# Performance work log

Measured on AMD Instinct MI355X. Metric: run time of the kernel, lower is better.

The kernel has to match this reference:

```python
import jax, jax.numpy as jnp
import numpy as np

THRESH = 0.3
DECAY = 0.5


def spike_fn(x):
    # Heaviside threshold (forward only)
    return (x > THRESH).astype(x.dtype)


def setup_inputs() -> dict:
    key = jax.random.key(0)
    k_in, k0, k1, k2 = jax.random.split(key, 4)
    B, D0, T = 128, 512, 512
    inputs = jax.random.uniform(k_in, (B, D0, T), dtype=jnp.float32)
    w0 = jax.random.normal(k0, (512, 1024), dtype=jnp.float32)
    w1 = jax.random.normal(k1, (1024, 1024), dtype=jnp.float32)
    w2 = jax.random.normal(k2, (1024, 512), dtype=jnp.float32)
    return {"inputs": inputs, "w0": w0, "w1": w1, "w2": w2}


def reference(inputs, w0, w1, w2):
    ws = (w0, w1, w2)
    B = inputs.shape[0]
    layer_dims = tuple(w.shape[1] for w in ws)

    # time-major: [T, B, D0]
    xs = jnp.transpose(inputs, (2, 0, 1))

    mem0 = tuple(jnp.zeros((B, d), dtype=inputs.dtype) for d in layer_dims)
    spk0 = tuple(jnp.zeros((B, d), dtype=inputs.dtype) for d in layer_dims)

    def step(carry, x_t):
        mems, spikes = carry
        prev_spike = x_t  # layer-0 spikes come straight from the input
        new_mems, new_spikes = [], []
        for i, w in enumerate(ws):
            # leaky integrate with reset-by-spike, then fire
            mem = mems[i] * DECAY * (1.0 - spikes[i]) + prev_spike @ w
            s = spike_fn(mem)
            new_mems.append(mem)
            new_spikes.append(s)
            prev_spike = s
        return (tuple(new_mems), tuple(new_spikes)), None

    (_, spikes_final), _ = jax.lax.scan(step, (mem0, spk0), xs)
    return spikes_final[-1]
```

## Files before the change

kernel.cpp:

```cpp
#include <hip/hip_runtime.h>


typedef __bf16 bf16;
typedef __attribute__((ext_vector_type(8))) __bf16 bf16x8;
typedef __attribute__((ext_vector_type(16))) float f32x16;
typedef unsigned long long u64;

#define B_   128
#define D0_  512
#define T_   512
#define TS_  128
#define N1_  1024
#define N2_  1024
#define N3_  512
#define MFMA32(a,b,c) __builtin_amdgcn_mfma_f32_32x32x16_bf16((a),(b),(c),0,0,0)

#define GL2LDS(g, l) __builtin_amdgcn_global_load_lds( \
    (const __attribute__((address_space(1))) void*)(g), \
    (__attribute__((address_space(3))) void*)(l), 16, 0, 0)

#define WAIT_BARRIER() do { \
    asm volatile("s_waitcnt vmcnt(0)" ::: "memory"); \
    __builtin_amdgcn_s_barrier(); } while (0)


__global__ __launch_bounds__(256)
void split_w(const float* __restrict__ W, bf16* __restrict__ WTh, bf16* __restrict__ WTl,
             int K, int N)
{
    __shared__ float tile[32][33];
    const int k0 = blockIdx.x * 32, n0 = blockIdx.y * 32;
    const int tx = threadIdx.x & 31, ty = threadIdx.x >> 5;
#pragma unroll
    for (int r = 0; r < 4; ++r)
        tile[ty + r * 8][tx] = W[(size_t)(k0 + ty + r * 8) * N + n0 + tx];
    __syncthreads();
#pragma unroll
    for (int r = 0; r < 4; ++r) {
        int nl = ty + r * 8;
        float v = tile[tx][nl];
        bf16 h = (bf16)v;
        size_t o = (size_t)(n0 + nl) * K + k0 + tx;
        WTh[o] = h;
        WTl[o] = (bf16)(v - (float)h);
    }
}

__global__ __launch_bounds__(64)
void split_wf(const float* __restrict__ W, bf16* __restrict__ Fh, bf16* __restrict__ Fl,
              int K, int N)
{
    const int l = threadIdx.x;
    const int kc = blockIdx.x;
    const int np = blockIdx.y;
    const int c  = np * 32 + (l & 31);
    const int k0 = kc * 16 + (l >> 5) * 8;
    const size_t ob = (((size_t)np * (K / 16) + kc) * 64 + l) * 8;
#pragma unroll
    for (int e = 0; e < 8; ++e) {
        float v = W[(size_t)(k0 + e) * N + c];
        bf16 h = (bf16)v;
        Fh[ob + e] = h;
        Fl[ob + e] = (bf16)(v - (float)h);
    }
}

__global__ __launch_bounds__(256)
void split_x(const float* __restrict__ in, bf16* __restrict__ Xh, bf16* __restrict__ Xl)
{
    __shared__ float tile[32][33];
    const int b = blockIdx.z, d0 = blockIdx.x * 32, t0 = blockIdx.y * 32;
    const int tx = threadIdx.x & 31, ty = threadIdx.x >> 5;
#pragma unroll
    for (int r = 0; r < 4; ++r)
        tile[ty + r * 8][tx] = in[((size_t)b * D0_ + d0 + ty + r * 8) * T_ + t0 + tx];
    __syncthreads();
    const int s = t0 >> 7;
#pragma unroll
    for (int r = 0; r < 4; ++r) {
        int t  = t0 + ty + r * 8;
        int tl = t & (TS_ - 1);
        float v = tile[tx][ty + r * 8];
        bf16 h = (bf16)v;
        size_t o = (((size_t)s * B_ + b) * TS_ + tl) * D0_ + d0 + tx;
        Xh[o] = h;
        Xl[o] = (bf16)(v - (float)h);
    }
}

__device__ __forceinline__ bf16x8 expand8(unsigned v)
{
    union { unsigned u[4]; bf16x8 h; } r;
    const unsigned p = v * 0x8001u;
#pragma unroll
    for (int i = 0; i < 4; ++i)
        r.u[i] = ((p >> (2 * i)) & 0x10001u) * 0x3F80u;
    return r.h;
}

__global__ __launch_bounds__(256, 2)
void snn_layer0(const bf16* __restrict__ Ah, const bf16* __restrict__ Al,
                const bf16* __restrict__ WTh, const bf16* __restrict__ WTl,
                u64* __restrict__ bitsOut)
{
    constexpr int K = D0_;
    __shared__ char smem[65536];
    bf16* sA0  = (bf16*)(smem);
    bf16* sAl0 = (bf16*)(smem + 8192);
    bf16* sB0  = (bf16*)(smem + 16384);
    bf16* sBl0 = (bf16*)(smem + 24576);
    bf16* sA1  = (bf16*)(smem + 32768);
    bf16* sAl1 = (bf16*)(smem + 40960);
    bf16* sB1  = (bf16*)(smem + 49152);
    bf16* sBl1 = (bf16*)(smem + 57344);
    float* If  = (float*)smem;

    const int tid = threadIdx.x, lane = tid & 63, w = tid >> 6;
    const int wm = w & 1, wn = w >> 1;
    const int l31 = lane & 31, kh = lane >> 5;
    const int bid = blockIdx.x;
    const int b  = (bid & 7) | ((bid >> 6) << 3);
    const int nb = ((bid >> 3) & 7) * 128;

    const int i4 = lane >> 2, c4 = lane & 3;
    const int csrc = c4 ^ ((i4 >> 1) & 3);
    const bf16* gBh = WTh + (size_t)(nb + w * 32 + i4) * K + csrc * 8;
    const bf16* gBl = WTl + (size_t)(nb + w * 32 + i4) * K + csrc * 8;
    const int wT = w * 32 * 32;

    int rA[2], rB[2], swA[2], swB[2];
#pragma unroll
    for (int i = 0; i < 2; ++i) {
        rA[i] = wm * 64 + i * 32 + l31;
        rB[i] = wn * 64 + i * 32 + l31;
        swA[i] = (rA[i] >> 1) & 3;
        swB[i] = (rB[i] >> 1) & 3;
    }

    float cm = 0.f, cs = 0.f;
    const int scol = tid & 63;
    float* Ifb = If + (tid >> 6) * 4096;

#define STAGE0(dA, dAl, dBh, dBl, go)                                          \
    do {                                                                       \
        _Pragma("unroll")                                                      \
        for (int inst = 0; inst < 2; ++inst) {                                 \
            GL2LDS(gA  + (size_t)(inst * 16) * K + (go), (dA)  + wT + inst * 16 * 32); \
            GL2LDS(gAl + (size_t)(inst * 16) * K + (go), (dAl) + wT + inst * 16 * 32); \
            GL2LDS(gBh + (size_t)(inst * 16) * K + (go), (dBh) + wT + inst * 16 * 32); \
            GL2LDS(gBl + (size_t)(inst * 16) * K + (go), (dBl) + wT + inst * 16 * 32); \
        }                                                                      \
    } while (0)

#define KSTEP0(cA, cAl, cBh, cBl)                                              \
    do {                                                                       \
        bf16x8 a[2][2], al2[2][2];                                             \
        _Pragma("unroll")                                                      \
        for (int mi = 0; mi < 2; ++mi)                                         \
            _Pragma("unroll")                                                  \
            for (int h = 0; h < 2; ++h) {                                      \
                const int off = rA[mi] * 32 + (((2 * h + kh) ^ swA[mi]) * 8);  \
                a[mi][h]   = *(const bf16x8*)((cA) + off);                     \
                al2[mi][h] = *(const bf16x8*)((cAl) + off);                    \
            }                                                                  \
        _Pragma("unroll")                                                      \
        for (int h = 0; h < 2; ++h) {                                          \
            bf16x8 bh[2], bl[2];                                               \
            _Pragma("unroll")                                                  \
            for (int ni = 0; ni < 2; ++ni) {                                   \
                const int off = rB[ni] * 32 + (((2 * h + kh) ^ swB[ni]) * 8);  \
                bh[ni] = *(const bf16x8*)((cBh) + off);                        \
                bl[ni] = *(const bf16x8*)((cBl) + off);                        \
            }                                                                  \
            _Pragma("unroll")                                                  \
            for (int ni = 0; ni < 2; ++ni)                                     \
                _Pragma("unroll")                                              \
                for (int mi = 0; mi < 2; ++mi)                                 \
                    acc[mi][ni] = MFMA32(a[mi][h], bh[ni], acc[mi][ni]);       \
            _Pragma("unroll")                                                  \
            for (int ni = 0; ni < 2; ++ni)                                     \
                _Pragma("unroll")                                              \
                for (int mi = 0; mi < 2; ++mi)                                 \
                    acc[mi][ni] = MFMA32(al2[mi][h], bh[ni], acc[mi][ni]);     \
            _Pragma("unroll")                                                  \
            for (int ni = 0; ni < 2; ++ni)                                     \
                _Pragma("unroll")                                              \
                for (int mi = 0; mi < 2; ++mi)                                 \
                    acc[mi][ni] = MFMA32(a[mi][h], bl[ni], acc[mi][ni]);       \
        }                                                                      \
        WAIT_BARRIER();                                                        \
    } while (0)

#pragma unroll 1
    for (int s = 0; s < T_ / TS_; ++s) {
        const size_t arow = ((size_t)s * B_ + b) * TS_;
        const bf16* gA  = Ah + (arow + w * 32 + i4) * K + csrc * 8;
        const bf16* gAl = Al + (arow + w * 32 + i4) * K + csrc * 8;

        STAGE0(sA0, sAl0, sB0, sBl0, 0);
        WAIT_BARRIER();

        f32x16 acc[2][2] = {};

#pragma unroll 1
        for (int ks = 0; ks < K / 32; ks += 2) {
            STAGE0(sA1, sAl1, sB1, sBl1, (ks + 1) * 32);
            KSTEP0(sA0, sAl0, sB0, sBl0);
            if (ks + 2 < K / 32)
                STAGE0(sA0, sAl0, sB0, sBl0, (ks + 2) * 32);
            KSTEP0(sA1, sAl1, sB1, sBl1);
        }

        u64 word0 = 0, word1 = 0;
        if (wm == 0) {
#pragma unroll
            for (int ni = 0; ni < 2; ++ni)
#pragma unroll
                for (int mi = 0; mi < 2; ++mi)
#pragma unroll
                    for (int r = 0; r < 16; ++r) {
                        const int tt = mi * 32 + (r & 3) + 8 * (r >> 2) + 4 * kh;
                        If[wn * 4096 + tt * 64 + ni * 32 + l31] = acc[mi][ni][r];
                    }
        }
        __syncthreads();
        if (tid < 128) {
            float m = cm, sp = cs;
#pragma unroll 4
            for (int tt = 0; tt < 64; ++tt) {
                m = m * 0.5f * (1.0f - sp) + Ifb[tt * 64 + scol];
                const bool fire = m > 0.3f;
                sp = fire ? 1.0f : 0.0f;
                u64 bal = __ballot(fire);
                if ((tid & 63) == tt) word0 = bal;
            }
            cm = m; cs = sp;
        }
        __syncthreads();
        if (wm == 1) {
#pragma unroll
            for (int ni = 0; ni < 2; ++ni)
#pragma unroll
                for (int mi = 0; mi < 2; ++mi)
#pragma unroll
                    for (int r = 0; r < 16; ++r) {
                        const int tt = mi * 32 + (r & 3) + 8 * (r >> 2) + 4 * kh;
                        If[wn * 4096 + tt * 64 + ni * 32 + l31] = acc[mi][ni][r];
                    }
        }
        __syncthreads();
        if (tid < 128) {
            float m = cm, sp = cs;
#pragma unroll 4
            for (int tt = 0; tt < 64; ++tt) {
                m = m * 0.5f * (1.0f - sp) + Ifb[tt * 64 + scol];
                const bool fire = m > 0.3f;
                sp = fire ? 1.0f : 0.0f;
                u64 bal = __ballot(fire);
                if ((tid & 63) == tt) word1 = bal;
            }
            cm = m; cs = sp;
            u64* dst = bitsOut + ((size_t)s * B_ + b) * 2048;
            const int j8 = (nb >> 6) + (tid >> 6);
            const int t0 = tid & 63, t1 = 64 + (tid & 63);
            dst[t0 * 16 + (j8 ^ (t0 & 15))] = word0;
            dst[t1 * 16 + (j8 ^ (t1 & 15))] = word1;
        }
        __syncthreads();
    }
#undef STAGE0
#undef KSTEP0
}

template<bool WRITE_BITS>
__global__ __launch_bounds__(256, 2)
void snn_layer_bits(const u64* __restrict__ bitsIn,
                    const bf16* __restrict__ WFh, const bf16* __restrict__ WFl,
                    u64* __restrict__ bitsOut, float* __restrict__ outp, int N)
{
    constexpr int K = 1024, KC = K / 16;
    __shared__ char smem[49152];
    char* bitsLds = smem;
    float* If = (float*)(smem + 16384);

    const int tid = threadIdx.x, lane = tid & 63, w = tid >> 6;
    const int wm = w & 1, wn = w >> 1;
    const int l31 = lane & 31, kh = lane >> 5;
    const int b = blockIdx.y;
    const int nb = blockIdx.x * 128;

    const size_t fb0 = ((size_t)((nb >> 5) + wn * 2) * KC) * 512 + (size_t)lane * 8;
    const size_t fb1 = fb0 + (size_t)KC * 512;
    const bf16* h0 = WFh + fb0;
    const bf16* h1 = WFh + fb1;
    const bf16* l0 = WFl + fb0;
    const bf16* l1 = WFl + fb1;

    const int sh8 = 8 * kh, s15 = l31 & 15;
    const int rA0b = (wm * 64 + l31) * 128;
    const int rA1b = (wm * 64 + 32 + l31) * 128;

    float cm = 0.f, cs = 0.f;
    const int scol = tid & 63;
    float* Ifb = If + (tid >> 6) * 4096;

#define LOADQ(sl, kc)                                                          \
    do {                                                                       \
        q0h[sl] = *(const bf16x8*)(h0 + (size_t)(kc) * 512);                   \
        q1h[sl] = *(const bf16x8*)(h1 + (size_t)(kc) * 512);                   \
        q0l[sl] = *(const bf16x8*)(l0 + (size_t)(kc) * 512);                   \
        q1l[sl] = *(const bf16x8*)(l1 + (size_t)(kc) * 512);                   \
    } while (0)

#define JSTEP(j, CB0, CB1)                                                     \
    do {                                                                       \
        bf16x8 a0 = expand8((unsigned)((CB0) >> (16 * (j) + sh8)) & 0xFFu);    \
        bf16x8 a1 = expand8((unsigned)((CB1) >> (16 * (j) + sh8)) & 0xFFu);    \
        acc[0][0] = MFMA32(a0, q0h[j], acc[0][0]);                             \
        acc[1][0] = MFMA32(a1, q0h[j], acc[1][0]);                             \
        acc[0][1] = MFMA32(a0, q1h[j], acc[0][1]);                             \
        acc[1][1] = MFMA32(a1, q1h[j], acc[1][1]);                             \
        acc[0][0] = MFMA32(a0, q0l[j], acc[0][0]);                             \
        acc[1][0] = MFMA32(a1, q0l[j], acc[1][0]);                             \
        acc[0][1] = MFMA32(a0, q1l[j], acc[0][1]);                             \
        acc[1][1] = MFMA32(a1, q1l[j], acc[1][1]);                             \
    } while (0)

#pragma unroll 1
    for (int s = 0; s < T_ / TS_; ++s) {
        {
            const char* src = (const char*)bitsIn + ((size_t)s * B_ + b) * 16384;
#pragma unroll
            for (int i = 0; i < 4; ++i)
                GL2LDS(src + (w * 4 + i) * 1024 + lane * 16,
                       bitsLds + (w * 4 + i) * 1024);
        }
        WAIT_BARRIER();

        f32x16 acc[2][2] = {};
        bf16x8 q0h[4], q0l[4], q1h[4], q1l[4];

        LOADQ(0, 0);
        LOADQ(1, 1);
        u64 cb0 = *(const u64*)(bitsLds + rA0b + ((0 ^ s15) << 3));
        u64 cb1 = *(const u64*)(bitsLds + rA1b + ((0 ^ s15) << 3));

#pragma unroll 1
        for (int pi = 0; pi < 15; ++pi) {
            const u64 nb0 = *(const u64*)(bitsLds + rA0b + (((pi + 1) ^ s15) << 3));
            const u64 nb1 = *(const u64*)(bitsLds + rA1b + (((pi + 1) ^ s15) << 3));
            const int kc = pi * 4;
            LOADQ(2, kc + 2); JSTEP(0, cb0, cb1);
            LOADQ(3, kc + 3); JSTEP(1, cb0, cb1);
            LOADQ(0, kc + 4); JSTEP(2, cb0, cb1);
            LOADQ(1, kc + 5); JSTEP(3, cb0, cb1);
            cb0 = nb0; cb1 = nb1;
        }
        LOADQ(2, 62); JSTEP(0, cb0, cb1);
        LOADQ(3, 63); JSTEP(1, cb0, cb1);
        JSTEP(2, cb0, cb1);
        JSTEP(3, cb0, cb1);

        u64 word0 = 0, word1 = 0;
        if (wm == 0) {
#pragma unroll
            for (int ni = 0; ni < 2; ++ni)
#pragma unroll
                for (int mi = 0; mi < 2; ++mi)
#pragma unroll
                    for (int r = 0; r < 16; ++r) {
                        const int tt = mi * 32 + (r & 3) + 8 * (r >> 2) + 4 * kh;
                        If[wn * 4096 + tt * 64 + ni * 32 + l31] = acc[mi][ni][r];
                    }
        }
        __syncthreads();
        if (tid < 128) {
            float m = cm, sp = cs;
#pragma unroll 4
            for (int tt = 0; tt < 64; ++tt) {
                m = m * 0.5f * (1.0f - sp) + Ifb[tt * 64 + scol];
                const bool fire = m > 0.3f;
                sp = fire ? 1.0f : 0.0f;
                if constexpr (WRITE_BITS) {
                    u64 bal = __ballot(fire);
                    if ((tid & 63) == tt) word0 = bal;
                }
            }
            cm = m; cs = sp;
        }
        __syncthreads();
        if (wm == 1) {
#pragma unroll
            for (int ni = 0; ni < 2; ++ni)
#pragma unroll
                for (int mi = 0; mi < 2; ++mi)
#pragma unroll
                    for (int r = 0; r < 16; ++r) {
                        const int tt = mi * 32 + (r & 3) + 8 * (r >> 2) + 4 * kh;
                        If[wn * 4096 + tt * 64 + ni * 32 + l31] = acc[mi][ni][r];
                    }
        }
        __syncthreads();
        if (tid < 128) {
            float m = cm, sp = cs;
#pragma unroll 4
            for (int tt = 0; tt < 64; ++tt) {
                m = m * 0.5f * (1.0f - sp) + Ifb[tt * 64 + scol];
                const bool fire = m > 0.3f;
                sp = fire ? 1.0f : 0.0f;
                if constexpr (WRITE_BITS) {
                    u64 bal = __ballot(fire);
                    if ((tid & 63) == tt) word1 = bal;
                }
            }
            cm = m; cs = sp;
            if constexpr (WRITE_BITS) {
                u64* dst = bitsOut + ((size_t)s * B_ + b) * 2048;
                const int j8 = (nb >> 6) + (tid >> 6);
                const int t0 = tid & 63, t1 = 64 + (tid & 63);
                dst[t0 * 16 + (j8 ^ (t0 & 15))] = word0;
                dst[t1 * 16 + (j8 ^ (t1 & 15))] = word1;
            } else {
                if (s == T_ / TS_ - 1)
                    outp[(size_t)b * N + nb + tid] = cs;
            }
        }
        __syncthreads();
    }
#undef LOADQ
#undef JSTEP
}

extern "C" void kernel_launch(void* const* d_in, const int* in_sizes, int n_in,
                              void* d_out, int out_size, void* d_ws, size_t ws_size,
                              hipStream_t stream)
{
    const float* x  = (const float*)d_in[0];
    const float* w0 = (const float*)d_in[1];
    const float* w1 = (const float*)d_in[2];
    const float* w2 = (const float*)d_in[3];
    float* out = (float*)d_out;

    char* p = (char*)d_ws;
    bf16* w0h  = (bf16*)p; p += (size_t)N1_ * D0_ * 2;
    bf16* w0l  = (bf16*)p; p += (size_t)N1_ * D0_ * 2;
    bf16* wf1h = (bf16*)p; p += (size_t)N2_ * N1_ * 2;
    bf16* wf1l = (bf16*)p; p += (size_t)N2_ * N1_ * 2;
    bf16* wf2h = (bf16*)p; p += (size_t)N3_ * N2_ * 2;
    bf16* wf2l = (bf16*)p; p += (size_t)N3_ * N2_ * 2;
    bf16* Xh   = (bf16*)p; p += (size_t)T_ * B_ * D0_ * 2;
    bf16* Xl   = (bf16*)p; p += (size_t)T_ * B_ * D0_ * 2;
    u64* bits0 = (u64*)p;  p += (size_t)(T_/TS_) * B_ * TS_ * (N1_/8);
    u64* bits1 = (u64*)p;  p += (size_t)(T_/TS_) * B_ * TS_ * (N2_/8);

    split_w<<<dim3(D0_/32, N1_/32), 256, 0, stream>>>(w0, w0h, w0l, D0_, N1_);
    split_wf<<<dim3(N1_/16, N2_/32), 64, 0, stream>>>(w1, wf1h, wf1l, N1_, N2_);
    split_wf<<<dim3(N2_/16, N3_/32), 64, 0, stream>>>(w2, wf2h, wf2l, N2_, N3_);
    split_x<<<dim3(D0_/32, T_/32, B_), 256, 0, stream>>>(x, Xh, Xl);

    snn_layer0<<<dim3(B_ * (N1_/128)), 256, 0, stream>>>(Xh, Xl, w0h, w0l, bits0);
    snn_layer_bits<true ><<<dim3(N2_/128, B_), 256, 0, stream>>>(
        bits0, wf1h, wf1l, bits1, nullptr, N2_);
    snn_layer_bits<false><<<dim3(N3_/128, B_), 256, 0, stream>>>(
        bits1, wf2h, wf2l, nullptr, out, N3_);
}
```

Baseline: 806.0 us.

## Pre-swizzle layer-0 operands into MFMA fragment layout and load directly to registers

The input and layer-0 weights are now split into bf16 hi/lo parts stored in MFMA-fragment order, so snn_layer0 reads each operand fragment straight from global memory into registers with a two-slot register double buffer. This removes the LDS staging, swizzled LDS reads and per-k-step barriers from the layer-0 GEMM. In exchange, operand tiles are no longer shared through LDS, so each wave loads its own fragments from global/L2. The new split_xf kernel reads the input with strided per-thread loads and may be slower than the old tiled transpose.

After: 795.1 us. About the same (-1.4%).

```diff
diff --git a/kernel.cpp b/kernel.cpp
--- a/kernel.cpp
+++ b/kernel.cpp
@@ -24,28 +24,6 @@
     __builtin_amdgcn_s_barrier(); } while (0)
 
 
-__global__ __launch_bounds__(256)
-void split_w(const float* __restrict__ W, bf16* __restrict__ WTh, bf16* __restrict__ WTl,
-             int K, int N)
-{
-    __shared__ float tile[32][33];
-    const int k0 = blockIdx.x * 32, n0 = blockIdx.y * 32;
-    const int tx = threadIdx.x & 31, ty = threadIdx.x >> 5;
-#pragma unroll
-    for (int r = 0; r < 4; ++r)
-        tile[ty + r * 8][tx] = W[(size_t)(k0 + ty + r * 8) * N + n0 + tx];
-    __syncthreads();
-#pragma unroll
-    for (int r = 0; r < 4; ++r) {
-        int nl = ty + r * 8;
-        float v = tile[tx][nl];
-        bf16 h = (bf16)v;
-        size_t o = (size_t)(n0 + nl) * K + k0 + tx;
-        WTh[o] = h;
-        WTl[o] = (bf16)(v - (float)h);
-    }
-}
-
 __global__ __launch_bounds__(64)
 void split_wf(const float* __restrict__ W, bf16* __restrict__ Fh, bf16* __restrict__ Fl,
               int K, int N)
@@ -65,26 +43,23 @@
     }
 }
 
-__global__ __launch_bounds__(256)
-void split_x(const float* __restrict__ in, bf16* __restrict__ Xh, bf16* __restrict__ Xl)
-{
-    __shared__ float tile[32][33];
-    const int b = blockIdx.z, d0 = blockIdx.x * 32, t0 = blockIdx.y * 32;
-    const int tx = threadIdx.x & 31, ty = threadIdx.x >> 5;
-#pragma unroll
-    for (int r = 0; r < 4; ++r)
-        tile[ty + r * 8][tx] = in[((size_t)b * D0_ + d0 + ty + r * 8) * T_ + t0 + tx];
-    __syncthreads();
-    const int s = t0 >> 7;
-#pragma unroll
-    for (int r = 0; r < 4; ++r) {
-        int t  = t0 + ty + r * 8;
-        int tl = t & (TS_ - 1);
-        float v = tile[tx][ty + r * 8];
+__global__ __launch_bounds__(64)
+void split_xf(const float* __restrict__ in, bf16* __restrict__ Fh, bf16* __restrict__ Fl)
+{
+    const int l  = threadIdx.x;
+    const int kc = blockIdx.x;
+    const int tb = blockIdx.y;
+    const int sb = blockIdx.z;
+    const int s = sb >> 7, b = sb & 127;
+    const int t  = s * TS_ + tb * 32 + (l & 31);
+    const int k0 = kc * 16 + (l >> 5) * 8;
+    const size_t ob = (((size_t)sb * 4 + tb) * 32 + kc) * 512 + (size_t)l * 8;
+#pragma unroll
+    for (int e = 0; e < 8; ++e) {
+        float v = in[((size_t)b * D0_ + k0 + e) * T_ + t];
         bf16 h = (bf16)v;
-        size_t o = (((size_t)s * B_ + b) * TS_ + tl) * D0_ + d0 + tx;
-        Xh[o] = h;
-        Xl[o] = (bf16)(v - (float)h);
+        Fh[ob + e] = h;
+        Fl[ob + e] = (bf16)(v - (float)h);
     }
 }
 
@@ -99,21 +74,12 @@
 }
 
 __global__ __launch_bounds__(256, 2)
-void snn_layer0(const bf16* __restrict__ Ah, const bf16* __restrict__ Al,
-                const bf16* __restrict__ WTh, const bf16* __restrict__ WTl,
+void snn_layer0(const bf16* __restrict__ XFh, const bf16* __restrict__ XFl,
+                const bf16* __restrict__ WFh, const bf16* __restrict__ WFl,
                 u64* __restrict__ bitsOut)
 {
-    constexpr int K = D0_;
-    __shared__ char smem[65536];
-    bf16* sA0  = (bf16*)(smem);
-    bf16* sAl0 = (bf16*)(smem + 8192);
-    bf16* sB0  = (bf16*)(smem + 16384);
-    bf16* sBl0 = (bf16*)(smem + 24576);
-    bf16* sA1  = (bf16*)(smem + 32768);
-    bf16* sAl1 = (bf16*)(smem + 40960);
-    bf16* sB1  = (bf16*)(smem + 49152);
-    bf16* sBl1 = (bf16*)(smem + 57344);
-    float* If  = (float*)smem;
+    constexpr int KC0 = D0_ / 16;
+    __shared__ float If[8192];
 
     const int tid = threadIdx.x, lane = tid & 63, w = tid >> 6;
     const int wm = w & 1, wn = w >> 1;
@@ -122,94 +88,67 @@
     const int b  = (bid & 7) | ((bid >> 6) << 3);
     const int nb = ((bid >> 3) & 7) * 128;
 
-    const int i4 = lane >> 2, c4 = lane & 3;
-    const int csrc = c4 ^ ((i4 >> 1) & 3);
-    const bf16* gBh = WTh + (size_t)(nb + w * 32 + i4) * K + csrc * 8;
-    const bf16* gBl = WTl + (size_t)(nb + w * 32 + i4) * K + csrc * 8;
-    const int wT = w * 32 * 32;
-
-    int rA[2], rB[2], swA[2], swB[2];
-#pragma unroll
-    for (int i = 0; i < 2; ++i) {
-        rA[i] = wm * 64 + i * 32 + l31;
-        rB[i] = wn * 64 + i * 32 + l31;
-        swA[i] = (rA[i] >> 1) & 3;
-        swB[i] = (rB[i] >> 1) & 3;
-    }
+    const size_t fb0 = ((size_t)((nb >> 5) + wn * 2) * KC0) * 512 + (size_t)lane * 8;
+    const bf16* b0h = WFh + fb0;
+    const bf16* b1h = b0h + (size_t)KC0 * 512;
+    const bf16* b0l = WFl + fb0;
+    const bf16* b1l = b0l + (size_t)KC0 * 512;
 
     float cm = 0.f, cs = 0.f;
     const int scol = tid & 63;
     float* Ifb = If + (tid >> 6) * 4096;
 
-#define STAGE0(dA, dAl, dBh, dBl, go)                                          \
+#define LOADF(sl, kc)                                                          \
     do {                                                                       \
-        _Pragma("unroll")                                                      \
-        for (int inst = 0; inst < 2; ++inst) {                                 \
-            GL2LDS(gA  + (size_t)(inst * 16) * K + (go), (dA)  + wT + inst * 16 * 32); \
-            GL2LDS(gAl + (size_t)(inst * 16) * K + (go), (dAl) + wT + inst * 16 * 32); \
-            GL2LDS(gBh + (size_t)(inst * 16) * K + (go), (dBh) + wT + inst * 16 * 32); \
-            GL2LDS(gBl + (size_t)(inst * 16) * K + (go), (dBl) + wT + inst * 16 * 32); \
-        }                                                                      \
+        qah[sl][0] = *(const bf16x8*)(a0h + (size_t)(kc) * 512);               \
+        qah[sl][1] = *(const bf16x8*)(a1h + (size_t)(kc) * 512);               \
+        qal[sl][0] = *(const bf16x8*)(a0l + (size_t)(kc) * 512);               \
+        qal[sl][1] = *(const bf16x8*)(a1l + (size_t)(kc) * 512);               \
+        qbh[sl][0] = *(const bf16x8*)(b0h + (size_t)(kc) * 512);               \
+        qbh[sl][1] = *(const bf16x8*)(b1h + (size_t)(kc) * 512);               \
+        qbl[sl][0] = *(const bf16x8*)(b0l + (size_t)(kc) * 512);               \
+        qbl[sl][1] = *(const bf16x8*)(b1l + (size_t)(kc) * 512);               \
     } while (0)
 
-#define KSTEP0(cA, cAl, cBh, cBl)                                              \
+#define COMPUTEF(sl)                                                           \
     do {                                                                       \
-        bf16x8 a[2][2], al2[2][2];                                             \
-        _Pragma("unroll")                                                      \
-        for (int mi = 0; mi < 2; ++mi)                                         \
-            _Pragma("unroll")                                                  \
-            for (int h = 0; h < 2; ++h) {                                      \
-                const int off = rA[mi] * 32 + (((2 * h + kh) ^ swA[mi]) * 8);  \
-                a[mi][h]   = *(const bf16x8*)((cA) + off);                     \
-                al2[mi][h] = *(const bf16x8*)((cAl) + off);                    \
-            }                                                                  \
-        _Pragma("unroll")                                                      \
-        for (int h = 0; h < 2; ++h) {                                          \
-            bf16x8 bh[2], bl[2];                                               \
-            _Pragma("unroll")                                                  \
-            for (int ni = 0; ni < 2; ++ni) {                                   \
-                const int off = rB[ni] * 32 + (((2 * h + kh) ^ swB[ni]) * 8);  \
-                bh[ni] = *(const bf16x8*)((cBh) + off);                        \
-                bl[ni] = *(const bf16x8*)((cBl) + off);                        \
-            }                                                                  \
-            _Pragma("unroll")                                                  \
-            for (int ni = 0; ni < 2; ++ni)                                     \
-                _Pragma("unroll")                                              \
-                for (int mi = 0; mi < 2; ++mi)                                 \
-                    acc[mi][ni] = MFMA32(a[mi][h], bh[ni], acc[mi][ni]);       \
-            _Pragma("unroll")                                                  \
-            for (int ni = 0; ni < 2; ++ni)                                     \
-                _Pragma("unroll")                                              \
-                for (int mi = 0; mi < 2; ++mi)                                 \
-                    acc[mi][ni] = MFMA32(al2[mi][h], bh[ni], acc[mi][ni]);     \
-            _Pragma("unroll")                                                  \
-            for (int ni = 0; ni < 2; ++ni)                                     \
-                _Pragma("unroll")                                              \
-                for (int mi = 0; mi < 2; ++mi)                                 \
-                    acc[mi][ni] = MFMA32(a[mi][h], bl[ni], acc[mi][ni]);       \
-        }                                                                      \
-        WAIT_BARRIER();                                                        \
+        acc[0][0] = MFMA32(qah[sl][0], qbh[sl][0], acc[0][0]);                 \
+        acc[1][0] = MFMA32(qah[sl][1], qbh[sl][0], acc[1][0]);                 \
+        acc[0][1] = MFMA32(qah[sl][0], qbh[sl][1], acc[0][1]);                 \
+        acc[1][1] = MFMA32(qah[sl][1], qbh[sl][1], acc[1][1]);                 \
+        acc[0][0] = MFMA32(qal[sl][0], qbh[sl][0], acc[0][0]);                 \
+        acc[1][0] = MFMA32(qal[sl][1], qbh[sl][0], acc[1][0]);                 \
+        acc[0][1] = MFMA32(qal[sl][0], qbh[sl][1], acc[0][1]);                 \
+        acc[1][1] = MFMA32(qal[sl][1], qbh[sl][1], acc[1][1]);                 \
+        acc[0][0] = MFMA32(qah[sl][0], qbl[sl][0], acc[0][0]);                 \
+        acc[1][0] = MFMA32(qah[sl][1], qbl[sl][0], acc[1][0]);                 \
+        acc[0][1] = MFMA32(qah[sl][0], qbl[sl][1], acc[0][1]);                 \
+        acc[1][1] = MFMA32(qah[sl][1], qbl[sl][1], acc[1][1]);                 \
     } while (0)
 
 #pragma unroll 1
     for (int s = 0; s < T_ / TS_; ++s) {
-        const size_t arow = ((size_t)s * B_ + b) * TS_;
-        const bf16* gA  = Ah + (arow + w * 32 + i4) * K + csrc * 8;
-        const bf16* gAl = Al + (arow + w * 32 + i4) * K + csrc * 8;
-
-        STAGE0(sA0, sAl0, sB0, sBl0, 0);
-        WAIT_BARRIER();
+        const size_t ab = ((size_t)(s * B_ + b) * 4 + wm * 2) * ((size_t)KC0 * 512)
+                          + (size_t)lane * 8;
+        const bf16* a0h = XFh + ab;
+        const bf16* a1h = a0h + (size_t)KC0 * 512;
+        const bf16* a0l = XFl + ab;
+        const bf16* a1l = a0l + (size_t)KC0 * 512;
 
         f32x16 acc[2][2] = {};
-
+        bf16x8 qah[2][2], qal[2][2], qbh[2][2], qbl[2][2];
+
+        LOADF(0, 0);
+        LOADF(1, 1);
 #pragma unroll 1
-        for (int ks = 0; ks < K / 32; ks += 2) {
-            STAGE0(sA1, sAl1, sB1, sBl1, (ks + 1) * 32);
-            KSTEP0(sA0, sAl0, sB0, sBl0);
-            if (ks + 2 < K / 32)
-                STAGE0(sA0, sAl0, sB0, sBl0, (ks + 2) * 32);
-            KSTEP0(sA1, sAl1, sB1, sBl1);
-        }
+        for (int kc = 0; kc < 30; kc += 2) {
+            COMPUTEF(0);
+            LOADF(0, kc + 2);
+            COMPUTEF(1);
+            LOADF(1, kc + 3);
+        }
+        COMPUTEF(0);
+        COMPUTEF(1);
 
         u64 word0 = 0, word1 = 0;
         if (wm == 0) {
@@ -268,8 +207,8 @@
         }
         __syncthreads();
     }
-#undef STAGE0
-#undef KSTEP0
+#undef LOADF
+#undef COMPUTEF
 }
 
 template<bool WRITE_BITS>
@@ -442,23 +381,23 @@
     float* out = (float*)d_out;
 
     char* p = (char*)d_ws;
-    bf16* w0h  = (bf16*)p; p += (size_t)N1_ * D0_ * 2;
-    bf16* w0l  = (bf16*)p; p += (size_t)N1_ * D0_ * 2;
+    bf16* wf0h = (bf16*)p; p += (size_t)N1_ * D0_ * 2;
+    bf16* wf0l = (bf16*)p; p += (size_t)N1_ * D0_ * 2;
     bf16* wf1h = (bf16*)p; p += (size_t)N2_ * N1_ * 2;
     bf16* wf1l = (bf16*)p; p += (size_t)N2_ * N1_ * 2;
     bf16* wf2h = (bf16*)p; p += (size_t)N3_ * N2_ * 2;
     bf16* wf2l = (bf16*)p; p += (size_t)N3_ * N2_ * 2;
-    bf16* Xh   = (bf16*)p; p += (size_t)T_ * B_ * D0_ * 2;
-    bf16* Xl   = (bf16*)p; p += (size_t)T_ * B_ * D0_ * 2;
+    bf16* XFh  = (bf16*)p; p += (size_t)T_ * B_ * D0_ * 2;
+    bf16* XFl  = (bf16*)p; p += (size_t)T_ * B_ * D0_ * 2;
     u64* bits0 = (u64*)p;  p += (size_t)(T_/TS_) * B_ * TS_ * (N1_/8);
     u64* bits1 = (u64*)p;  p += (size_t)(T_/TS_) * B_ * TS_ * (N2_/8);
 
-    split_w<<<dim3(D0_/32, N1_/32), 256, 0, stream>>>(w0, w0h, w0l, D0_, N1_);
+    split_wf<<<dim3(D0_/16, N1_/32), 64, 0, stream>>>(w0, wf0h, wf0l, D0_, N1_);
     split_wf<<<dim3(N1_/16, N2_/32), 64, 0, stream>>>(w1, wf1h, wf1l, N1_, N2_);
     split_wf<<<dim3(N2_/16, N3_/32), 64, 0, stream>>>(w2, wf2h, wf2l, N2_, N3_);
-    split_x<<<dim3(D0_/32, T_/32, B_), 256, 0, stream>>>(x, Xh, Xl);
-
-    snn_layer0<<<dim3(B_ * (N1_/128)), 256, 0, stream>>>(Xh, Xl, w0h, w0l, bits0);
+    split_xf<<<dim3(32, 4, (T_/TS_) * B_), 64, 0, stream>>>(x, XFh, XFl);
+
+    snn_layer0<<<dim3(B_ * (N1_/128)), 256, 0, stream>>>(XFh, XFl, wf0h, wf0l, bits0);
     snn_layer_bits<true ><<<dim3(N2_/128, B_), 256, 0, stream>>>(
         bits0, wf1h, wf1l, bits1, nullptr, N2_);
     snn_layer_bits<false><<<dim3(N3_/128, B_), 256, 0, stream>>>(
```
